# Optimization experiments

Measured on AMD Instinct MI355X. Metric: run time of the kernel, lower is better.

Reference implementation:

```python
import jax, jax.numpy as jnp
import numpy as np

D, R, C = 4, 6, 32
P = 2 * R + 1          # 13 (both pixel patch and memory patch, since memory_patch_R == R)
N = P * P              # 169
DIL_INT = 15


def corr_sampler(f1, f2, p, dil):
    """SpatialCorrelationSampler(kernel_size=1, patch_size=p, dilation_patch=dil).
    out[b,i,j,y,x] = sum_c f1[b,c,y,x] * f2[b,c, y+(i-Rp)*dil, x+(j-Rp)*dil] (zero pad)."""
    Rp = (p - 1) // 2
    pad = Rp * dil
    b, c, h, w = f1.shape
    f2p = jnp.pad(f2, ((0, 0), (0, 0), (pad, pad), (pad, pad)))
    outs = [jnp.einsum('bchw,bchw->bhw', f1, f2p[:, :, i * dil:i * dil + h, j * dil:j * dil + w])
            for i in range(p) for j in range(p)]
    return jnp.stack(outs, 1).reshape(b, p, p, h, w)


def bilinear_gather(im, ys, xs):
    """Bilinear sample im [b,c,H,W] at float coords ys,xs [b,N,h,w]; zeros outside."""
    H, W = im.shape[2], im.shape[3]
    y0 = jnp.floor(ys)
    x0 = jnp.floor(xs)
    wy = ys - y0
    wx = xs - x0

    def g(yi, xi):
        valid = ((yi >= 0) & (yi < H) & (xi >= 0) & (xi < W)).astype(im.dtype)
        yc = jnp.clip(yi, 0, H - 1).astype(jnp.int32)
        xc = jnp.clip(xi, 0, W - 1).astype(jnp.int32)
        out = jax.vmap(lambda imb, yb, xb: imb[:, yb, xb])(im, yc, xc)  # [b,c,N,h,w]
        return out * valid[:, None]

    return (g(y0, x0) * ((1 - wy) * (1 - wx))[:, None]
            + g(y0, x0 + 1) * ((1 - wy) * wx)[:, None]
            + g(y0 + 1, x0) * (wy * (1 - wx))[:, None]
            + g(y0 + 1, x0 + 1) * (wy * wx)[:, None])


def deform_im2col(im, offset, p):
    """Deformable im2col: for each output pixel (y,x) and kernel pos (ky,kx),
    bilinearly sample im at (y+ky-Rp+off_y, x+kx-Rp+off_x). offset [...,0]=x, [...,1]=y.
    Returns [b,c,p*p,h,w]."""
    b, c, h, w = im.shape
    Rp = (p - 1) // 2
    ky, kx = jnp.meshgrid(jnp.arange(p) - Rp, jnp.arange(p) - Rp, indexing='ij')
    ky = ky.reshape(-1).astype(im.dtype)
    kx = kx.reshape(-1).astype(im.dtype)
    ys = (jnp.arange(h, dtype=im.dtype)[None, None, :, None]
          + ky[None, :, None, None] + offset[..., 1][:, None])  # [b,N,h,w]
    xs = (jnp.arange(w, dtype=im.dtype)[None, None, None, :]
          + kx[None, :, None, None] + offset[..., 0][:, None])
    return bilinear_gather(im, ys, xs)


def unfold_patches(x, p, pad):
    """F.unfold(kernel_size=p, padding=pad) -> [b,c,p*p,h,w]."""
    b, c, h, w = x.shape
    xp = jnp.pad(x, ((0, 0), (0, 0), (pad, pad), (pad, pad)))
    cols = [xp[:, :, i:i + h, j:j + w] for i in range(p) for j in range(p)]
    return jnp.stack(cols, 2)


def _forward(feats_r, feats_t, quantized_r, ref_index, current_ind):
    ri = np.asarray(ref_index)
    ci = int(current_ind)
    diffs = [ci - int(x) for x in ri]
    nsearch = sum(1 for d in diffs if d > DIL_INT)
    dirates = [min(4, d // DIL_INT + 1) for d in diffs if d > DIL_INT]
    nref = feats_r.shape[0]
    b, c, h, w = feats_t.shape

    # offset grid: _y,_x = meshgrid(ij) so grid[...,0]=x-offset, grid[...,1]=y-offset
    _y, _x = jnp.meshgrid(jnp.arange(-R, R + 1), jnp.arange(-R, R + 1), indexing='ij')
    grid = jnp.stack([_x, _y], -1).astype(feats_t.dtype)  # [P,P,2]

    corrs_pixel = []
    offset0 = []
    for s in range(nsearch):
        cc = corr_sampler(feats_t, feats_r[s], P, dirates[s])             # [b,P,P,h,w]
        soft = jax.nn.softmax(cc.reshape(b, N, h * w), axis=1).reshape(b, P, P, h, w)
        off = jnp.einsum('bijhw,ijd->bhwd', soft, grid) * dirates[s]      # [b,h,w,2]
        offset0.append(off)
        col0 = deform_im2col(feats_r[s], off, P)                          # [b,c,N,h,w]
        corrs_pixel.append(jnp.einsum('bchw,bcnhw->bnhw', feats_t, col0).reshape(b, N, h * w))
    for ind in range(nsearch, nref):
        corrs_pixel.append(corr_sampler(feats_t, feats_r[ind], P, 1).reshape(b, N, h * w))

    corr_pixel = jax.nn.softmax(jnp.concatenate(corrs_pixel, 1), axis=1)  # [b,nref*N,h*w]

    # prep: float + stride-D subsampling (C-channel input, so no one-hot branch)
    qr = [quantized_r[i][:, :, ::D, ::D] for i in range(nref)]            # [b,C,h,w]
    cols = [deform_im2col(qr[i], offset0[i], P).reshape(b, C, N, h * w) for i in range(nsearch)]
    cols += [unfold_patches(qr[i], P, R).reshape(b, C, N, h * w) for i in range(nsearch, nref)]
    image_uf = jnp.concatenate(cols, 2)                                   # [b,C,nref*N,h*w]

    out = jnp.einsum('bkl,bckl->bcl', corr_pixel, image_uf).reshape(b, C, h, w)
    return out


def setup_inputs() -> dict:
    key = jax.random.key(0)
    k1, k2, k3 = jax.random.split(key, 3)
    feats_r = jax.random.normal(k1, (3, 1, 64, 56, 56), jnp.float32) * 0.2
    feats_t = jax.random.normal(k2, (1, 64, 56, 56), jnp.float32) * 0.2
    quantized_r = jax.random.uniform(k3, (3, 1, 32, 224, 224), jnp.float32)
    return {
        'feats_r': feats_r,
        'feats_t': feats_t,
        'quantized_r': quantized_r,
        'ref_index': np.array([0, 30, 39], dtype=np.int64),
        'current_ind': 40,
    }


def reference(feats_r, feats_t, quantized_r, ref_index, current_ind):
    return _forward(feats_r, feats_t, quantized_r, ref_index, current_ind)
```

## Files before the change

### kernel.cpp

```cpp
#include <hip/hip_runtime.h>

#define HW    56
#define NPIX  3136
#define CH    64
#define CQ    32
#define PS    13
#define NPOS  169
#define GS    14
#define NG    196
#define G1    15
#define NG1   225

typedef __attribute__((ext_vector_type(8))) short short8;
typedef __attribute__((ext_vector_type(4))) float f32x4;

__device__ inline ushort f2bf(float f) {
  unsigned u = __float_as_uint(f);
  return (ushort)((u + 0x7fffu + ((u >> 16) & 1u)) >> 16);
}
__device__ inline float bf2f(ushort u) {
  return __uint_as_float((unsigned)u << 16);
}
__device__ inline void wave_sync() {
  asm volatile("s_waitcnt lgkmcnt(0)" ::: "memory");
  __builtin_amdgcn_sched_barrier(0);
}

__global__ __launch_bounds__(256) void prep_all(
    const float* __restrict__ ft_in,
    const float* __restrict__ fr_in,
    const float* __restrict__ q_in,
    ushort* __restrict__ ft_out,
    ushort* __restrict__ fr_out,
    ushort* __restrict__ qout,
    float* __restrict__ zrow) {
  __shared__ float smem[CQ * (HW + 1)];
  int bid = blockIdx.x, tid = threadIdx.x;
  if (bid < 784) {
    if (bid == 0 && tid < 64) zrow[tid] = 0.f;
    int m = bid / 196, t = bid - m * 196;
    int row0 = (t / 98) * 32;
    int col0 = (t - (t / 98) * 98) * 32;
    const float* src = (m == 0) ? ft_in : fr_in + (size_t)(m - 1) * CH * NPIX;
    ushort* dst      = (m == 0) ? ft_out : fr_out + (size_t)(m - 1) * NPIX * CH;
    int tx = tid & 31, ty = tid >> 5;
    for (int r = ty; r < 32; r += 8)
      smem[r * 33 + tx] = src[(size_t)(row0 + r) * NPIX + col0 + tx];
    __syncthreads();
    for (int r = ty; r < 32; r += 8)
      dst[(size_t)(col0 + r) * CH + row0 + tx] = f2bf(smem[tx * 33 + r]);
  } else {
    int q = bid - 784;
    int r = q / HW, yy = q - r * HW;
    for (int idx = tid; idx < CQ * HW; idx += 256) {
      int c = idx / HW, xx = idx - c * HW;
      smem[c * (HW + 1) + xx] = q_in[((size_t)(r * CQ + c) * 224 + yy * 4) * 224 + xx * 4];
    }
    __syncthreads();
    for (int idx = tid; idx < CQ * HW; idx += 256) {
      int xx = idx >> 5, c = idx & 31;
      qout[(size_t)r * NPIX * CQ + (size_t)(yy * HW + xx) * CQ + c] = f2bf(smem[c * (HW + 1) + xx]);
    }
  }
}

__global__ __launch_bounds__(256, 4) void colorizer_main(
    const ushort* __restrict__ ftb,
    const ushort* __restrict__ frb,
    const ushort* __restrict__ qrb,
    const ushort* __restrict__ zrow,
    float* __restrict__ out)
{
  __shared__ float C1[1024];
  __shared__ float C2[1024];
  __shared__ int   pw[4 * 832];
  __shared__ float m2s[4], Sas[4];
  __shared__ float fqr0[128];
  __shared__ float red2[512];

  int tid = threadIdx.x;
  int wid = tid >> 6, lane = tid & 63;
  int mrow = lane & 15, klane = lane >> 4;

  int bx = blockIdx.x % 28, by = blockIdx.x / 28;
  int Y0 = by * 2, X0 = bx * 2;
  int dy = wid >> 1, dx = wid & 1;
  int y = Y0 + dy, x = X0 + dx;
  int pix = y * HW + x;

  int*   wb   = pw + wid * 832;
  float* e    = (float*)wb;
  float* D    = (float*)(wb + 176);
  float* wg   = (float*)(wb + 384);
  int*   offg = wb + 608;
  float* cc   = (float*)offg;

  if (lane < 16) offg[208 + lane] = -1;

  const ushort* frb0 = frb;
  const ushort* frb1 = frb + (size_t)NPIX * CH;
  const ushort* frb2 = frb + (size_t)2 * NPIX * CH;
  const ushort* qr0b = qrb;
  const ushort* qr1b = qrb + (size_t)NPIX * CQ;
  const ushort* qr2b = qrb + (size_t)2 * NPIX * CQ;

  const ushort* fb = ftb + (size_t)pix * CH;
  const ushort* plo = (mrow == 0) ? (fb + klane * 8) : zrow;
  const ushort* phi = (mrow == 0) ? (fb + 32 + klane * 8) : zrow;
  short8 b_lo = *(const short8*)plo;
  short8 b_hi = *(const short8*)phi;

  const ushort* fb4 = (mrow < 4)
      ? (ftb + (size_t)((Y0 + (mrow >> 1)) * HW + X0 + (mrow & 1)) * CH)
      : zrow;
  short8 b4_lo = *(const short8*)(fb4 + klane * 8);
  short8 b4_hi = *(const short8*)(fb4 + 32 + klane * 8);

#pragma unroll
  for (int k = 0; k < 8; ++k) {
    int j = wid + 4 * k;
    if (j < 30) {
      int r = (j >= 15);
      int t = j - r * 15;
      int g = t * 16 + mrow;
      int gy = g / G1, gx = g - gy * G1;
      int sy = Y0 - 6 + gy, sx = X0 - 6 + gx;
      bool v = (g < NG1) && ((unsigned)sy < HW) && ((unsigned)sx < HW);
      const ushort* base = r ? frb2 : frb1;
      const ushort* rb = v ? (base + (size_t)(sy * HW + sx) * CH) : zrow;
      short8 alo = *(const short8*)(rb + klane * 8);
      short8 ahi = *(const short8*)(rb + 32 + klane * 8);
      f32x4 acc = {0.f, 0.f, 0.f, 0.f};
      acc = __builtin_amdgcn_mfma_f32_16x16x32_bf16(alo, b4_lo, acc, 0, 0, 0);
      acc = __builtin_amdgcn_mfma_f32_16x16x32_bf16(ahi, b4_hi, acc, 0, 0, 0);
      int col = lane & 15;
      if (col < 4) {
        float* Cd = r ? C2 : C1;
        int row0 = t * 16 + (lane >> 4) * 4;
#pragma unroll
        for (int q = 0; q < 4; ++q) Cd[(row0 + q) * 4 + col] = acc[q];
      }
    }
  }
  __syncthreads();

#pragma unroll
  for (int g = 0; g < 11; ++g) {
    int d = g * 16 + mrow;
    int ii = d / PS, jj = d - ii * PS;
    int sy = y + (ii - 6) * 3, sx = x + (jj - 6) * 3;
    bool v = (d < NPOS) && ((unsigned)sy < HW) && ((unsigned)sx < HW);
    const ushort* rb = v ? (frb0 + (size_t)(sy * HW + sx) * CH) : zrow;
    short8 alo = *(const short8*)(rb + klane * 8);
    short8 ahi = *(const short8*)(rb + 32 + klane * 8);
    f32x4 acc = {0.f, 0.f, 0.f, 0.f};
    acc = __builtin_amdgcn_mfma_f32_16x16x32_bf16(alo, b_lo, acc, 0, 0, 0);
    acc = __builtin_amdgcn_mfma_f32_16x16x32_bf16(ahi, b_hi, acc, 0, 0, 0);
    if (mrow == 0) *(f32x4*)&cc[g * 16 + klane * 4] = acc;
  }
  wave_sync();

  float vs[3];
  float mx = -1e30f;
#pragma unroll
  for (int k = 0; k < 3; ++k) {
    int id = lane + 64 * k;
    float c = (id < NPOS) ? cc[id] : -1e30f;
    vs[k] = c;
    mx = fmaxf(mx, c);
  }
#pragma unroll
  for (int o = 1; o < 64; o <<= 1) mx = fmaxf(mx, __shfl_xor(mx, o));
  float se = 0.f, sxe = 0.f, sye = 0.f;
#pragma unroll
  for (int k = 0; k < 3; ++k) {
    int id = lane + 64 * k;
    if (id < NPOS) {
      float ex = __expf(vs[k] - mx);
      int pi = id / PS, pj = id - pi * PS;
      se += ex;
      sxe += ex * (float)(pj - 6);
      sye += ex * (float)(pi - 6);
    }
  }
#pragma unroll
  for (int o = 1; o < 64; o <<= 1) {
    se  += __shfl_xor(se, o);
    sxe += __shfl_xor(sxe, o);
    sye += __shfl_xor(sye, o);
  }
  float offx = 3.f * sxe / se;
  float offy = 3.f * sye / se;

  float fy0 = floorf(offy), fx0 = floorf(offx);
  int   iy0 = (int)fy0,     ix0 = (int)fx0;
  float wyf = offy - fy0,   wxf = offx - fx0;
  float w00 = (1.f - wyf) * (1.f - wxf), w01 = (1.f - wyf) * wxf;
  float w10 = wyf * (1.f - wxf),         w11 = wyf * wxf;

#pragma unroll
  for (int g = 0; g < 13; ++g) {
    int d = g * 16 + mrow;
    int a = d / GS, bq = d - a * GS;
    int sy = y + iy0 + a - 6, sx = x + ix0 + bq - 6;
    bool vA = (d < NG) && ((unsigned)sy < HW) && ((unsigned)sx < HW);
    int roA = sy * HW + sx;
    const ushort* rbA = vA ? (frb0 + (size_t)roA * CH) : zrow;
    short8 aAlo = *(const short8*)(rbA + klane * 8);
    short8 aAhi = *(const short8*)(rbA + 32 + klane * 8);
    f32x4 accA = {0.f, 0.f, 0.f, 0.f};
    accA = __builtin_amdgcn_mfma_f32_16x16x32_bf16(aAlo, b_lo, accA, 0, 0, 0);
    accA = __builtin_amdgcn_mfma_f32_16x16x32_bf16(aAhi, b_hi, accA, 0, 0, 0);
    if (klane == 0) offg[d] = vA ? roA : -1;
    if (mrow == 0) *(f32x4*)&D[g * 16 + klane * 4] = accA;
  }
  wave_sync();

#pragma unroll
  for (int k = 0; k < 3; ++k) {
    int id = lane + 64 * k;
    if (id < NPOS) {
      int pi = id / PS, pj = id - (id / PS) * PS;
      e[id] = w00 * D[pi * GS + pj]       + w01 * D[pi * GS + pj + 1]
            + w10 * D[(pi + 1) * GS + pj] + w11 * D[(pi + 1) * GS + pj + 1];
    } else if (id < 176) {
      e[id] = -1e30f;
    }
  }
  wave_sync();

  float mx2 = -1e30f;
#pragma unroll
  for (int k = 0; k < 3; ++k) {
    int id = lane + 64 * k;
    if (id < 176) mx2 = fmaxf(mx2, e[id]);
    if (id < NPOS) {
      int ii = id / PS, jj = id - (id / PS) * PS;
      int g = (ii + dy) * G1 + (jj + dx);
      mx2 = fmaxf(mx2, fmaxf(C1[g * 4 + wid], C2[g * 4 + wid]));
    }
  }
#pragma unroll
  for (int o = 1; o < 64; o <<= 1) mx2 = fmaxf(mx2, __shfl_xor(mx2, o));
  float ps = 0.f;
#pragma unroll
  for (int k = 0; k < 3; ++k) {
    int id = lane + 64 * k;
    if (id < 176) {
      float ex = __expf(e[id] - mx2);
      e[id] = ex;
      ps += ex;
    }
    if (id < NPOS) {
      int ii = id / PS, jj = id - (id / PS) * PS;
      int g = (ii + dy) * G1 + (jj + dx);
      ps += __expf(C1[g * 4 + wid] - mx2) + __expf(C2[g * 4 + wid] - mx2);
    }
  }
#pragma unroll
  for (int o = 1; o < 64; o <<= 1) ps += __shfl_xor(ps, o);
  if (lane == 0) { m2s[wid] = mx2; Sas[wid] = ps; }
  wave_sync();

#pragma unroll
  for (int k = 0; k < 4; ++k) {
    int t = lane + 64 * k;
    if (t < 224) {
      float acc = 0.f;
      if (t < NG) {
        int a = t / GS, b = t - (t / GS) * GS;
        if (a < PS && b < PS) acc += w00 * e[a * PS + b];
        if (a < PS && b >= 1) acc += w01 * e[a * PS + b - 1];
        if (a >= 1 && b < PS) acc += w10 * e[(a - 1) * PS + b];
        if (a >= 1 && b >= 1) acc += w11 * e[(a - 1) * PS + b - 1];
      }
      wg[t] = acc;
    }
  }
  wave_sync();

  int slot = lane >> 3, ln = lane & 7;
  f32x4 acc0 = {0.f, 0.f, 0.f, 0.f};
#pragma unroll
  for (int k = 0; k < 28; ++k) {
    int d = slot + k * 8;
    int ro = offg[d];
    if (ro >= 0) {
      float w = wg[d];
      ushort4 u = *(const ushort4*)(qr0b + (size_t)ro * CQ + ln * 4);
      acc0.x = fmaf(w, bf2f(u.x), acc0.x);
      acc0.y = fmaf(w, bf2f(u.y), acc0.y);
      acc0.z = fmaf(w, bf2f(u.z), acc0.z);
      acc0.w = fmaf(w, bf2f(u.w), acc0.w);
    }
  }
#pragma unroll
  for (int o = 8; o <= 32; o <<= 1) {
    acc0.x += __shfl_xor(acc0.x, o);
    acc0.y += __shfl_xor(acc0.y, o);
    acc0.z += __shfl_xor(acc0.z, o);
    acc0.w += __shfl_xor(acc0.w, o);
  }
  if (lane < 8) {
    fqr0[wid * 32 + lane * 4 + 0] = acc0.x;
    fqr0[wid * 32 + lane * 4 + 1] = acc0.y;
    fqr0[wid * 32 + lane * 4 + 2] = acc0.z;
    fqr0[wid * 32 + lane * 4 + 3] = acc0.w;
  }
  __syncthreads();

#pragma unroll
  for (int t = 0; t < 8; ++t) {
    int idx = tid + t * 256;
    int ref = idx >> 10;
    int ix = idx & 1023;
    int g = ix >> 2, p = ix & 3;
    int gy = g / G1, gx = g - gy * G1;
    int ii = gy - (p >> 1), jj = gx - (p & 1);
    bool win = (g < NG1) && ((unsigned)ii < PS) && ((unsigned)jj < PS);
    float* Cd = ref ? C2 : C1;
    float val = Cd[ix];
    Cd[ix] = win ? __expf(val - m2s[p]) : 0.f;
  }
  __syncthreads();

  int q8 = tid & 7, s = tid >> 3;
  float a12[4][4];
#pragma unroll
  for (int p = 0; p < 4; ++p)
#pragma unroll
    for (int c = 0; c < 4; ++c) a12[p][c] = 0.f;
#pragma unroll
  for (int i = 0; i < 8; ++i) {
    int g = s + 32 * i;
    if (g < NG1) {
      int gy = g / G1, gx = g - gy * G1;
      int sy = Y0 - 6 + gy, sx = X0 - 6 + gx;
      if (((unsigned)sy < HW) && ((unsigned)sx < HW)) {
        size_t ro = (size_t)(sy * HW + sx) * CQ + q8 * 4;
        ushort4 u1 = *(const ushort4*)(qr1b + ro);
        ushort4 u2 = *(const ushort4*)(qr2b + ro);
        f32x4 w1 = *(f32x4*)&C1[g * 4];
        f32x4 w2 = *(f32x4*)&C2[g * 4];
        float q1[4] = {bf2f(u1.x), bf2f(u1.y), bf2f(u1.z), bf2f(u1.w)};
        float q2[4] = {bf2f(u2.x), bf2f(u2.y), bf2f(u2.z), bf2f(u2.w)};
#pragma unroll
        for (int p = 0; p < 4; ++p)
#pragma unroll
          for (int c = 0; c < 4; ++c)
            a12[p][c] += w1[p] * q1[c] + w2[p] * q2[c];
      }
    }
  }
#pragma unroll
  for (int o = 8; o <= 32; o <<= 1)
#pragma unroll
    for (int p = 0; p < 4; ++p)
#pragma unroll
      for (int c = 0; c < 4; ++c)
        a12[p][c] += __shfl_xor(a12[p][c], o);
  if (lane < 8) {
#pragma unroll
    for (int p = 0; p < 4; ++p)
#pragma unroll
      for (int c = 0; c < 4; ++c)
        red2[wid * 128 + lane * 16 + p * 4 + c] = a12[p][c];
  }
  __syncthreads();

  if (tid < 128) {
    int p = tid >> 5, c = tid & 31;
    float tot = fqr0[p * 32 + c];
#pragma unroll
    for (int w = 0; w < 4; ++w)
      tot += red2[w * 128 + (c >> 2) * 16 + p * 4 + (c & 3)];
    int pidx = (Y0 + (p >> 1)) * HW + X0 + (p & 1);
    out[(size_t)c * NPIX + pidx] = tot / Sas[p];
  }
}

extern "C" void kernel_launch(void* const* d_in, const int* in_sizes, int n_in,
                              void* d_out, int out_size, void* d_ws, size_t ws_size,
                              hipStream_t stream) {
  const float* feats_r     = (const float*)d_in[0];
  const float* feats_t     = (const float*)d_in[1];
  const float* quantized_r = (const float*)d_in[2];

  ushort* ftb = (ushort*)d_ws;
  ushort* frb = ftb + 200704;
  ushort* qrb = frb + 602112;
  float*  zro = (float*)(qrb + 301056);

  prep_all<<<952, 256, 0, stream>>>(feats_t, feats_r, quantized_r,
                                    ftb, frb, qrb, zro);
  colorizer_main<<<784, 256, 0, stream>>>(ftb, frb, qrb, (const ushort*)zro,
                                          (float*)d_out);
}
```

Baseline: 45.80 us.

## Store softmax weights during reduction, widen loads, swizzle blocks, vectorize transpose

The softmax pass now writes the exponentiated correlation weights into new shared arrays W1/W2. This removes the separate full-block exp/mask pass over C1/C2 and one __syncthreads. The final aggregation and the ref-0 gather switch to 8-wide bf16 loads, with threads split across the two references, which changes the reduction layout in red2. Blocks are swizzled to change the tile visiting order, and the prep transpose uses vectorized float4 and ushort4 accesses. In exchange, shared memory use grows by about 12KB per block, which may reduce occupancy, and the wider a12 accumulators add register pressure.

```diff
diff --git a/kernel.cpp b/kernel.cpp
--- a/kernel.cpp
+++ b/kernel.cpp
@@ -12,6 +12,7 @@
 #define NG1   225
 
 typedef __attribute__((ext_vector_type(8))) short short8;
+typedef __attribute__((ext_vector_type(8))) ushort ushort8;
 typedef __attribute__((ext_vector_type(4))) float f32x4;
 
 __device__ inline ushort f2bf(float f) {
@@ -43,12 +44,17 @@
     int col0 = (t - (t / 98) * 98) * 32;
     const float* src = (m == 0) ? ft_in : fr_in + (size_t)(m - 1) * CH * NPIX;
     ushort* dst      = (m == 0) ? ft_out : fr_out + (size_t)(m - 1) * NPIX * CH;
-    int tx = tid & 31, ty = tid >> 5;
-    for (int r = ty; r < 32; r += 8)
-      smem[r * 33 + tx] = src[(size_t)(row0 + r) * NPIX + col0 + tx];
+    int ty = tid >> 3, tx4 = (tid & 7) * 4;
+    f32x4 v = *(const f32x4*)&src[(size_t)(row0 + ty) * NPIX + col0 + tx4];
+    *(f32x4*)&smem[ty * 33 + tx4] = v;
     __syncthreads();
-    for (int r = ty; r < 32; r += 8)
-      dst[(size_t)(col0 + r) * CH + row0 + tx] = f2bf(smem[tx * 33 + r]);
+    int px = tid >> 3, c4 = (tid & 7) * 4;
+    ushort4 o;
+    o.x = f2bf(smem[(c4 + 0) * 33 + px]);
+    o.y = f2bf(smem[(c4 + 1) * 33 + px]);
+    o.z = f2bf(smem[(c4 + 2) * 33 + px]);
+    o.w = f2bf(smem[(c4 + 3) * 33 + px]);
+    *(ushort4*)&dst[(size_t)(col0 + px) * CH + row0 + c4] = o;
   } else {
     int q = bid - 784;
     int r = q / HW, yy = q - r * HW;
@@ -73,16 +79,20 @@
 {
   __shared__ float C1[1024];
   __shared__ float C2[1024];
+  __shared__ float W1[1024];
+  __shared__ float W2[1024];
   __shared__ int   pw[4 * 832];
-  __shared__ float m2s[4], Sas[4];
+  __shared__ float Sas[4];
   __shared__ float fqr0[128];
-  __shared__ float red2[512];
+  __shared__ float red2[1024];
 
   int tid = threadIdx.x;
   int wid = tid >> 6, lane = tid & 63;
   int mrow = lane & 15, klane = lane >> 4;
 
-  int bx = blockIdx.x % 28, by = blockIdx.x / 28;
+  int b = blockIdx.x;
+  int swz = (b & 7) * 98 + (b >> 3);
+  int bx = swz % 28, by = swz / 28;
   int Y0 = by * 2, X0 = bx * 2;
   int dy = wid >> 1, dx = wid & 1;
   int y = Y0 + dy, x = X0 + dx;
@@ -96,6 +106,8 @@
   float* cc   = (float*)offg;
 
   if (lane < 16) offg[208 + lane] = -1;
+#pragma unroll
+  for (int k = 0; k < 4; ++k) { W1[tid + 256 * k] = 0.f; W2[tid + 256 * k] = 0.f; }
 
   const ushort* frb0 = frb;
   const ushort* frb1 = frb + (size_t)NPIX * CH;
@@ -254,12 +266,16 @@
     if (id < NPOS) {
       int ii = id / PS, jj = id - (id / PS) * PS;
       int g = (ii + dy) * G1 + (jj + dx);
-      ps += __expf(C1[g * 4 + wid] - mx2) + __expf(C2[g * 4 + wid] - mx2);
+      float e1c = __expf(C1[g * 4 + wid] - mx2);
+      float e2c = __expf(C2[g * 4 + wid] - mx2);
+      W1[g * 4 + wid] = e1c;
+      W2[g * 4 + wid] = e2c;
+      ps += e1c + e2c;
     }
   }
 #pragma unroll
   for (int o = 1; o < 64; o <<= 1) ps += __shfl_xor(ps, o);
-  if (lane == 0) { m2s[wid] = mx2; Sas[wid] = ps; }
+  if (lane == 0) Sas[wid] = ps;
   wave_sync();
 
 #pragma unroll
@@ -268,112 +284,95 @@
     if (t < 224) {
       float acc = 0.f;
       if (t < NG) {
-        int a = t / GS, b = t - (t / GS) * GS;
-        if (a < PS && b < PS) acc += w00 * e[a * PS + b];
-        if (a < PS && b >= 1) acc += w01 * e[a * PS + b - 1];
-        if (a >= 1 && b < PS) acc += w10 * e[(a - 1) * PS + b];
-        if (a >= 1 && b >= 1) acc += w11 * e[(a - 1) * PS + b - 1];
+        int a = t / GS, bq2 = t - (t / GS) * GS;
+        if (a < PS && bq2 < PS) acc += w00 * e[a * PS + bq2];
+        if (a < PS && bq2 >= 1) acc += w01 * e[a * PS + bq2 - 1];
+        if (a >= 1 && bq2 < PS) acc += w10 * e[(a - 1) * PS + bq2];
+        if (a >= 1 && bq2 >= 1) acc += w11 * e[(a - 1) * PS + bq2 - 1];
       }
       wg[t] = acc;
     }
   }
   wave_sync();
 
-  int slot = lane >> 3, ln = lane & 7;
-  f32x4 acc0 = {0.f, 0.f, 0.f, 0.f};
-#pragma unroll
-  for (int k = 0; k < 28; ++k) {
-    int d = slot + k * 8;
+  int slot = lane >> 2, ln4 = lane & 3;
+  float acc8[8];
+#pragma unroll
+  for (int c = 0; c < 8; ++c) acc8[c] = 0.f;
+#pragma unroll
+  for (int k = 0; k < 14; ++k) {
+    int d = slot + k * 16;
     int ro = offg[d];
     if (ro >= 0) {
       float w = wg[d];
-      ushort4 u = *(const ushort4*)(qr0b + (size_t)ro * CQ + ln * 4);
-      acc0.x = fmaf(w, bf2f(u.x), acc0.x);
-      acc0.y = fmaf(w, bf2f(u.y), acc0.y);
-      acc0.z = fmaf(w, bf2f(u.z), acc0.z);
-      acc0.w = fmaf(w, bf2f(u.w), acc0.w);
-    }
-  }
-#pragma unroll
-  for (int o = 8; o <= 32; o <<= 1) {
-    acc0.x += __shfl_xor(acc0.x, o);
-    acc0.y += __shfl_xor(acc0.y, o);
-    acc0.z += __shfl_xor(acc0.z, o);
-    acc0.w += __shfl_xor(acc0.w, o);
-  }
-  if (lane < 8) {
-    fqr0[wid * 32 + lane * 4 + 0] = acc0.x;
-    fqr0[wid * 32 + lane * 4 + 1] = acc0.y;
-    fqr0[wid * 32 + lane * 4 + 2] = acc0.z;
-    fqr0[wid * 32 + lane * 4 + 3] = acc0.w;
+      ushort8 u = *(const ushort8*)(qr0b + (size_t)ro * CQ + ln4 * 8);
+#pragma unroll
+      for (int c = 0; c < 8; ++c) acc8[c] = fmaf(w, bf2f(u[c]), acc8[c]);
+    }
+  }
+#pragma unroll
+  for (int o = 4; o <= 32; o <<= 1)
+#pragma unroll
+    for (int c = 0; c < 8; ++c) acc8[c] += __shfl_xor(acc8[c], o);
+  if (lane < 4) {
+#pragma unroll
+    for (int c = 0; c < 8; ++c) fqr0[wid * 32 + lane * 8 + c] = acc8[c];
   }
   __syncthreads();
 
-#pragma unroll
-  for (int t = 0; t < 8; ++t) {
-    int idx = tid + t * 256;
-    int ref = idx >> 10;
-    int ix = idx & 1023;
-    int g = ix >> 2, p = ix & 3;
-    int gy = g / G1, gx = g - gy * G1;
-    int ii = gy - (p >> 1), jj = gx - (p & 1);
-    bool win = (g < NG1) && ((unsigned)ii < PS) && ((unsigned)jj < PS);
-    float* Cd = ref ? C2 : C1;
-    float val = Cd[ix];
-    Cd[ix] = win ? __expf(val - m2s[p]) : 0.f;
-  }
-  __syncthreads();
-
-  int q8 = tid & 7, s = tid >> 3;
-  float a12[4][4];
-#pragma unroll
-  for (int p = 0; p < 4; ++p)
-#pragma unroll
-    for (int c = 0; c < 4; ++c) a12[p][c] = 0.f;
-#pragma unroll
-  for (int i = 0; i < 8; ++i) {
-    int g = s + 32 * i;
-    if (g < NG1) {
-      int gy = g / G1, gx = g - gy * G1;
-      int sy = Y0 - 6 + gy, sx = X0 - 6 + gx;
-      if (((unsigned)sy < HW) && ((unsigned)sx < HW)) {
-        size_t ro = (size_t)(sy * HW + sx) * CQ + q8 * 4;
-        ushort4 u1 = *(const ushort4*)(qr1b + ro);
-        ushort4 u2 = *(const ushort4*)(qr2b + ro);
-        f32x4 w1 = *(f32x4*)&C1[g * 4];
-        f32x4 w2 = *(f32x4*)&C2[g * 4];
-        float q1[4] = {bf2f(u1.x), bf2f(u1.y), bf2f(u1.z), bf2f(u1.w)};
-        float q2[4] = {bf2f(u2.x), bf2f(u2.y), bf2f(u2.z), bf2f(u2.w)};
-#pragma unroll
-        for (int p = 0; p < 4; ++p)
-#pragma unroll
-          for (int c = 0; c < 4; ++c)
-            a12[p][c] += w1[p] * q1[c] + w2[p] * q2[c];
+  {
+    int s = tid >> 3, ref = (tid >> 2) & 1, h = tid & 3;
+    const ushort* qb = ref ? qr2b : qr1b;
+    const float*  Wr = ref ? W2 : W1;
+    float a12[4][8];
+#pragma unroll
+    for (int p = 0; p < 4; ++p)
+#pragma unroll
+      for (int c = 0; c < 8; ++c) a12[p][c] = 0.f;
+#pragma unroll
+    for (int i = 0; i < 8; ++i) {
+      int g = s + 32 * i;
+      if (g < NG1) {
+        int gy = g / G1, gx = g - gy * G1;
+        int sy = Y0 - 6 + gy, sx = X0 - 6 + gx;
+        if (((unsigned)sy < HW) && ((unsigned)sx < HW)) {
+          ushort8 u = *(const ushort8*)(qb + (size_t)(sy * HW + sx) * CQ + h * 8);
+          f32x4 wv = *(const f32x4*)&Wr[g * 4];
+          float qv[8];
+#pragma unroll
+          for (int c = 0; c < 8; ++c) qv[c] = bf2f(u[c]);
+#pragma unroll
+          for (int p = 0; p < 4; ++p)
+#pragma unroll
+            for (int c = 0; c < 8; ++c) a12[p][c] = fmaf(wv[p], qv[c], a12[p][c]);
+        }
       }
     }
-  }
-#pragma unroll
-  for (int o = 8; o <= 32; o <<= 1)
-#pragma unroll
-    for (int p = 0; p < 4; ++p)
-#pragma unroll
-      for (int c = 0; c < 4; ++c)
-        a12[p][c] += __shfl_xor(a12[p][c], o);
-  if (lane < 8) {
-#pragma unroll
-    for (int p = 0; p < 4; ++p)
-#pragma unroll
-      for (int c = 0; c < 4; ++c)
-        red2[wid * 128 + lane * 16 + p * 4 + c] = a12[p][c];
+#pragma unroll
+    for (int o = 8; o <= 32; o <<= 1)
+#pragma unroll
+      for (int p = 0; p < 4; ++p)
+#pragma unroll
+        for (int c = 0; c < 8; ++c) a12[p][c] += __shfl_xor(a12[p][c], o);
+    if (lane < 8) {
+      int rh = lane;
+#pragma unroll
+      for (int p = 0; p < 4; ++p)
+#pragma unroll
+        for (int c = 0; c < 8; ++c)
+          red2[wid * 256 + rh * 32 + p * 8 + c] = a12[p][c];
+    }
   }
   __syncthreads();
 
   if (tid < 128) {
     int p = tid >> 5, c = tid & 31;
+    int h = c >> 3, c8 = c & 7;
     float tot = fqr0[p * 32 + c];
 #pragma unroll
     for (int w = 0; w < 4; ++w)
-      tot += red2[w * 128 + (c >> 2) * 16 + p * 4 + (c & 3)];
+      tot += red2[w * 256 + (0 * 4 + h) * 32 + p * 8 + c8]
+           + red2[w * 256 + (1 * 4 + h) * 32 + p * 8 + c8];
     int pidx = (Y0 + (p >> 1)) * HW + X0 + (p & 1);
     out[(size_t)c * NPIX + pidx] = tot / Sas[p];
   }
```

Measured after the change: 48.76 us. 1.06x slower.
